# Kernel tuning notes

Hardware: AMD Instinct MI355X
Metric: run time of the kernel (lower is better)

## Reference

```python
import jax, jax.numpy as jnp
import numpy as np

B, L = 4096, 64
H, E, T, S = 512, 256, 256, 128
CT = T + 3            # context feature dim (term_embedding_dim + 3)
R, V = 4096, 256      # n production rules, n symbols
IN = 2 * E + 2 * T + 6 + H + S  # GRUCell input dim = 1670
NEG = -1e9


def setup_inputs() -> dict:
    key = jax.random.key(0)
    ks = jax.random.split(key, 24)
    sc = 0.02
    inp = {
        "s_tm1": jax.random.normal(ks[0], (B, H), jnp.float32),
        "a_tm1": jax.random.normal(ks[1], (B, E), jnp.float32),
        "p_t": jax.random.normal(ks[2], (B, H + E), jnp.float32),
        "symbol_idx": jax.random.randint(ks[3], (B,), 0, V, jnp.int32),
        "env_emb": jax.random.normal(ks[4], (B, L, CT), jnp.float32),
        "env_len": jax.random.randint(ks[5], (B,), 0, L, jnp.int32),
        "lc_emb": jax.random.normal(ks[6], (B, L, CT), jnp.float32),
        "lc_len": jax.random.randint(ks[7], (B,), 0, L, jnp.int32),
        # parameters
        "symbol_table": jax.random.normal(ks[8], (V, S), jnp.float32) * sc,
        "W1": jax.random.normal(ks[9], (H + CT, H), jnp.float32) * sc,
        "b1": jnp.zeros((H,), jnp.float32),
        "W2": jax.random.normal(ks[10], (H,), jnp.float32) * sc,
        "b2": jnp.zeros((), jnp.float32),
        "W_ih": jax.random.normal(ks[11], (IN, 3 * H), jnp.float32) * sc,
        "W_hh": jax.random.normal(ks[12], (H, 3 * H), jnp.float32) * sc,
        "b_ih": jnp.zeros((3 * H,), jnp.float32),
        "b_hh": jnp.zeros((3 * H,), jnp.float32),
        "Wd": jax.random.normal(ks[13], (H, E), jnp.float32) * sc,
        "bd": jnp.zeros((E,), jnp.float32),
        "rule_table": jax.random.normal(ks[14], (R, E), jnp.float32) * sc,
    }
    return inp


def _context_read(state, emb, length, W1, b1, W2, b2):
    # state: [B,H], emb: [B,L,CT], length: [B] -> context [B,CT]
    x = jnp.concatenate([jnp.broadcast_to(state[:, None, :], emb.shape[:2] + (state.shape[-1],)), emb], axis=-1)
    h = jax.nn.relu(jnp.einsum('blk,kh->blh', x, W1) + b1)      # [B,L,H]
    logit = jnp.einsum('blh,h->bl', h, W2) + b2                  # [B,L]
    mask = jnp.arange(emb.shape[1])[None, :] < length[:, None]
    logit = jnp.where(mask, logit, NEG)
    w = jax.nn.softmax(logit, axis=1)                            # [B,L]
    ctx = jnp.einsum('bl,blc->bc', w, emb)                       # [B,CT]
    # ragged empty-context samples use the zero default_context
    return jnp.where((length > 0)[:, None], ctx, 0.0)


def reference(s_tm1, a_tm1, p_t, symbol_idx, env_emb, env_len, lc_emb, lc_len,
              symbol_table, W1, b1, W2, b2, W_ih, W_hh, b_ih, b_hh, Wd, bd, rule_table):
    n_t = symbol_table[symbol_idx]                               # [B,S]
    ctx_env = _context_read(s_tm1, env_emb, env_len, W1, b1, W2, b2)
    ctx_lc = _context_read(s_tm1, lc_emb, lc_len, W1, b1, W2, b2)
    x = jnp.concatenate([a_tm1, p_t, n_t, ctx_env, ctx_lc], axis=-1)  # [B,IN]
    # torch GRUCell
    gx = x @ W_ih + b_ih                                         # [B,3H]
    gh = s_tm1 @ W_hh + b_hh
    xr, xz, xn = jnp.split(gx, 3, axis=-1)
    hr, hz, hn = jnp.split(gh, 3, axis=-1)
    r = jax.nn.sigmoid(xr + hr)
    z = jax.nn.sigmoid(xz + hz)
    n = jnp.tanh(xn + r * hn)
    h_new = (1.0 - z) * n + z * s_tm1                            # [B,H]
    dec = jnp.tanh(h_new @ Wd + bd)                              # [B,E]
    logits = dec @ rule_table.T                                  # [B,R]
    return logits
```

## Files before the change

kernel.cpp:

```cpp
#include <hip/hip_runtime.h>
#include <hip/hip_bf16.h>
#include <stdint.h>
#include <stddef.h>

#define XP 1696
#define KC 288
#define EP 264

#define BIG_G   8192
#define TWO_G   4096
#define ONE_G   2048
#define N_GROUP (BIG_G + TWO_G + ONE_G)
#define N_SLOTI (N_GROUP * 4)

typedef __attribute__((ext_vector_type(8))) short bf16x8;
typedef __attribute__((ext_vector_type(4))) float f32x4;

__device__ __forceinline__ unsigned short f32_bf16(float f) {
    union { float f; unsigned int u; } v; v.f = f;
    unsigned int r = v.u + 0x7FFFu + ((v.u >> 16) & 1u);
    return (unsigned short)(r >> 16);
}
__device__ __forceinline__ unsigned int bf_rnd(float f) {
    union { float f; unsigned int u; } v; v.f = f;
    return v.u + 0x7FFFu + ((v.u >> 16) & 1u);
}
__device__ __forceinline__ float bf16_f32(unsigned short u) {
    union { unsigned int u; float f; } v; v.u = ((unsigned int)u) << 16;
    return v.f;
}

__global__ void tpack_kernel(const float* __restrict__ src, unsigned short* __restrict__ dst,
                             int Ksrc, int Nsrc, int Kp) {
    __shared__ float t[64][65];
    const int tid = threadIdx.x;
    const int n0 = blockIdx.x * 64, k0 = blockIdx.y * 64;
    const int ln = tid & 63;
    const int g  = tid >> 6;
    #pragma unroll
    for (int j = 0; j < 16; j++) {
        int kl = g + j * 4;
        int k = k0 + kl, n = n0 + ln;
        float v = 0.f;
        if (k < Ksrc && n < Nsrc) v = src[(size_t)k * Nsrc + n];
        t[kl][ln] = v;
    }
    __syncthreads();
    #pragma unroll
    for (int j = 0; j < 16; j++) {
        int nl = g + j * 4;
        int n = n0 + nl, k = k0 + ln;
        if (n < Nsrc && k < Kp) dst[(size_t)n * Kp + k] = f32_bf16(t[ln][nl]);
    }
}

__global__ void cvt_kernel(const float* __restrict__ src, unsigned short* __restrict__ dst, int total) {
    int idx = blockIdx.x * blockDim.x + threadIdx.x;
    if (idx < total) dst[idx] = f32_bf16(src[idx]);
}

__global__ void xasm_kernel(const float* __restrict__ a_tm1, const float* __restrict__ p_t,
                            const int* __restrict__ sym, const float* __restrict__ symtab,
                            unsigned short* __restrict__ x_out) {
    int idx = blockIdx.x * blockDim.x + threadIdx.x;
    if (idx >= 4096 * XP) return;
    int b = idx / XP, c = idx - b * XP;
    float v;
    if (c < 256)       v = a_tm1[(size_t)b * 256 + c];
    else if (c < 1024) v = p_t[(size_t)b * 768 + (c - 256)];
    else if (c < 1152) v = symtab[(size_t)sym[b] * 128 + (c - 1024)];
    else if (c < 1670) return;
    else v = 0.0f;
    x_out[idx] = f32_bf16(v);
}

__global__ void sinit_kernel(int* __restrict__ s) {
    int i = blockIdx.x * 256 + threadIdx.x;
    if (i < N_SLOTI) s[i] = -1;
    else if (i < N_SLOTI + 3) s[i] = 0;
}

__global__ void sched_kernel(const int* __restrict__ len_env, const int* __restrict__ len_lc,
                             int* __restrict__ slots) {
    int idx = blockIdx.x * blockDim.x + threadIdx.x;
    if (idx >= 8192) return;
    int b = idx >> 1, wh = idx & 1;
    int len = wh ? len_lc[b] : len_env[b];
    int m = (len + 15) >> 4;
    if (m == 0) m = 1;
    if (m > 4) m = 4;
    int* cursors = slots + N_SLOTI;
    int base;
    if (m >= 3)      { int p = atomicAdd(&cursors[0], 1); base = p * 4; }
    else if (m == 2) { int p = atomicAdd(&cursors[1], 1); base = BIG_G * 4 + (p >> 1) * 4 + (p & 1) * 2; }
    else             { int p = atomicAdd(&cursors[2], 1); base = (BIG_G + TWO_G) * 4 + (p >> 2) * 4 + (p & 3); }
    for (int k = 0; k < m; k++) slots[base + k] = idx * 4 + k;
}

template<int ACT, int OUT_BF16>
__global__ __launch_bounds__(256, 2)
void gemm_bt_kernel(const unsigned short* __restrict__ A,
                    const unsigned short* __restrict__ BT,
                    const float* __restrict__ bias,
                    void* __restrict__ Cout,
                    int M, int N, int K)
{
    __shared__ unsigned short a_lds[128 * 32];
    __shared__ unsigned short b_lds[128 * 32];
    const int tid  = threadIdx.x;
    const int lane = tid & 63;
    const int wave = tid >> 6;
    const int wm = wave >> 1, wn = wave & 1;
    const int row0 = blockIdx.y * 128;
    const int col0 = blockIdx.x * 128;

    f32x4 acc[4][4];
    #pragma unroll
    for (int i = 0; i < 4; i++)
        #pragma unroll
        for (int j = 0; j < 4; j++) acc[i][j] = (f32x4){0.f, 0.f, 0.f, 0.f};

    const int fr = lane & 15;
    const int kk = (lane >> 4) * 8;
    const int srow = (lane >> 2);
    const int scol = (lane & 3) * 8;

    for (int k0 = 0; k0 < K; k0 += 32) {
        __syncthreads();
        #pragma unroll
        for (int j = 0; j < 4; j++) {
            const int c = (wave & 1) * 4 + j;
            const unsigned short* gsrc;
            unsigned short* ldst;
            if (wave < 2) {
                gsrc = A  + (size_t)(row0 + c * 16 + srow) * K + k0 + scol;
                ldst = &a_lds[c * 512];
            } else {
                gsrc = BT + (size_t)(col0 + c * 16 + srow) * K + k0 + scol;
                ldst = &b_lds[c * 512];
            }
            __builtin_amdgcn_global_load_lds(
                (const __attribute__((address_space(1))) void*)gsrc,
                (__attribute__((address_space(3))) void*)ldst, 16, 0, 0);
        }
        __syncthreads();

        bf16x8 af[4], bf[4];
        #pragma unroll
        for (int mt = 0; mt < 4; mt++) af[mt] = *(const bf16x8*)&a_lds[(wm * 64 + mt * 16 + fr) * 32 + kk];
        #pragma unroll
        for (int nt = 0; nt < 4; nt++) bf[nt] = *(const bf16x8*)&b_lds[(wn * 64 + nt * 16 + fr) * 32 + kk];
        #pragma unroll
        for (int mt = 0; mt < 4; mt++)
            #pragma unroll
            for (int nt = 0; nt < 4; nt++)
                acc[mt][nt] = __builtin_amdgcn_mfma_f32_16x16x32_bf16(af[mt], bf[nt], acc[mt][nt], 0, 0, 0);
    }

    const int fq = lane >> 4;
    #pragma unroll
    for (int mt = 0; mt < 4; mt++)
        #pragma unroll
        for (int nt = 0; nt < 4; nt++) {
            int cg = col0 + wn * 64 + nt * 16 + fr;
            float bv = bias ? bias[cg] : 0.0f;
            #pragma unroll
            for (int i = 0; i < 4; i++) {
                int rg = row0 + wm * 64 + mt * 16 + fq * 4 + i;
                float v = acc[mt][nt][i] + bv;
                if (ACT == 1) v = tanhf(v);
                if (OUT_BF16) ((unsigned short*)Cout)[(size_t)rg * N + cg] = f32_bf16(v);
                else          ((float*)Cout)[(size_t)rg * N + cg] = v;
            }
        }
}

__global__ __launch_bounds__(512, 4)
void ctx_kernel(const float* __restrict__ emb_env, const float* __restrict__ emb_lc,
                const int* __restrict__ len_env, const int* __restrict__ len_lc,
                const float* __restrict__ s_proj,
                const unsigned short* __restrict__ W1eT,
                const float* __restrict__ W2, const float* __restrict__ b2,
                const int* __restrict__ slots,
                unsigned short* __restrict__ x_out)
{
    const int g = blockIdx.x;
    const int4 dv = *reinterpret_cast<const int4*>(slots + (size_t)g * 4);
    if (dv.x < 0) return;
    int d[4] = {dv.x, dv.y, dv.z, dv.w};

    __shared__ unsigned short emb_lds[64 * EP];
    __shared__ float partial_lds[8][64];
    __shared__ float w_lds[64];
    __shared__ int hinfo0[4], hinfo1[4], hinfo_n;

    const int tid = threadIdx.x;
    const int lane = tid & 63;
    const int wave = tid >> 6;
    const int fr = lane & 15;
    const int fq = lane >> 4;
    const float b2v = b2[0];

    if (tid == 0) {
        int n = 0;
        #pragma unroll
        for (int s = 0; s < 4; s++) {
            int dh = d[s];
            if (dh >= 0 && (dh & 3) == 0) {
                int it = dh >> 2;
                int b = it >> 1, wh = it & 1;
                int len = (wh ? len_lc : len_env)[b];
                hinfo0[n] = (s * 16) | (len << 8);
                hinfo1[n] = b * 2 + wh;
                n++;
            }
        }
        hinfo_n = n;
    }

    if (tid < 320) {
        int r = tid / 5, c = 259 + (tid - (tid / 5) * 5);
        emb_lds[r * EP + c] = 0;
    }

    {
        const int sl = tid >> 7;
        const int t  = tid & 127;
        const int ds = d[sl];
        int nrows = 0;
        const float* src = nullptr;
        if (ds >= 0) {
            int it = ds >> 2, tix = ds & 3;
            int b = it >> 1, wh = it & 1;
            int len = (wh ? len_lc : len_env)[b];
            nrows = len - tix * 16;
            if (nrows > 16) nrows = 16;
            if (nrows < 0) nrows = 0;
            src = (wh ? emb_lc : emb_env) + ((size_t)b * 64 + tix * 16) * 259;
        }
        const int nf4 = (nrows * 259 + 3) >> 2;
        const float4* s4 = reinterpret_cast<const float4*>(src);
        float4 v[9];
        #pragma unroll
        for (int j = 0; j < 9; j++) {
            int q = t + j * 128;
            if (q < nf4) v[j] = s4[q];
        }
        unsigned short* ebase = &emb_lds[sl * 16 * EP];
        #pragma unroll
        for (int j = 0; j < 9; j++) {
            int q = t + j * 128;
            if (q < nf4) {
                int e0 = q * 4;
                int r  = (int)(((unsigned)e0 * 64779u) >> 24);
                int c0 = e0 - r * 259;
                unsigned int u0 = bf_rnd(v[j].x), u1 = bf_rnd(v[j].y);
                unsigned int u2 = bf_rnd(v[j].z), u3 = bf_rnd(v[j].w);
                unsigned short* rp = ebase + r * EP;
                if (c0 <= 255) {
                    if ((c0 & 1) == 0) {
                        *(unsigned int*)(rp + c0)     = __builtin_amdgcn_perm(u1, u0, 0x07060302);
                        *(unsigned int*)(rp + c0 + 2) = __builtin_amdgcn_perm(u3, u2, 0x07060302);
                    } else {
                        rp[c0]     = (unsigned short)(u0 >> 16);
                        *(unsigned int*)(rp + c0 + 1) = __builtin_amdgcn_perm(u2, u1, 0x07060302);
                        rp[c0 + 3] = (unsigned short)(u3 >> 16);
                    }
                } else {
                    unsigned int uu[4] = {u0, u1, u2, u3};
                    #pragma unroll
                    for (int jj = 0; jj < 4; jj++) {
                        int e = e0 + jj;
                        int r2 = r, c2 = c0 + jj;
                        if (c2 >= 259) { r2 = r + 1; c2 -= 259; }
                        ebase[r2 * EP + c2] = (unsigned short)(uu[jj] >> 16);
                    }
                }
            }
        }
    }
    __syncthreads();

    f32x4 acc[4][4];
    #pragma unroll
    for (int i = 0; i < 4; i++)
        #pragma unroll
        for (int j = 0; j < 4; j++) acc[i][j] = (f32x4){0.f, 0.f, 0.f, 0.f};

    #pragma unroll
    for (int ks = 0; ks < 9; ks++) {
        bf16x8 bfr[4];
        #pragma unroll
        for (int nt = 0; nt < 4; nt++) {
            int n = wave * 64 + nt * 16 + fr;
            bfr[nt] = *(const bf16x8*)(W1eT + (size_t)n * KC + ks * 32 + fq * 8);
        }
        bf16x8 af[4];
        if (ks < 8) {
            #pragma unroll
            for (int mt = 0; mt < 4; mt++)
                af[mt] = *(const bf16x8*)&emb_lds[(mt * 16 + fr) * EP + ks * 32 + fq * 8];
        } else {
            #pragma unroll
            for (int mt = 0; mt < 4; mt++) {
                bf16x8 z = {};
                if (fq == 0) z = *(const bf16x8*)&emb_lds[(mt * 16 + fr) * EP + 256];
                af[mt] = z;
            }
        }
        __builtin_amdgcn_s_setprio(1);
        #pragma unroll
        for (int nt = 0; nt < 4; nt++)
            #pragma unroll
            for (int mt = 0; mt < 4; mt++)
                acc[mt][nt] = __builtin_amdgcn_mfma_f32_16x16x32_bf16(af[mt], bfr[nt], acc[mt][nt], 0, 0, 0);
        __builtin_amdgcn_s_setprio(0);
    }

    int bslot[4];
    #pragma unroll
    for (int mt = 0; mt < 4; mt++) bslot[mt] = d[mt] >= 0 ? (d[mt] >> 3) : -1;

    float wv[4];
    #pragma unroll
    for (int nt = 0; nt < 4; nt++) wv[nt] = W2[wave * 64 + nt * 16 + fr];

    float plog[4][4];
    #pragma unroll
    for (int mt = 0; mt < 4; mt++)
        #pragma unroll
        for (int ii = 0; ii < 4; ii++) plog[mt][ii] = 0.f;
    #pragma unroll
    for (int nt = 0; nt < 4; nt++) {
        int n = wave * 64 + nt * 16 + fr;
        #pragma unroll
        for (int mt = 0; mt < 4; mt++) {
            if (bslot[mt] < 0) continue;
            float sp = s_proj[(size_t)bslot[mt] * 512 + n];
            #pragma unroll
            for (int ii = 0; ii < 4; ii++) {
                float h = acc[mt][nt][ii] + sp;
                h = fmaxf(h, 0.f);
                plog[mt][ii] += h * wv[nt];
            }
        }
    }
    #pragma unroll
    for (int mt = 0; mt < 4; mt++) {
        if (bslot[mt] < 0) continue;
        #pragma unroll
        for (int ii = 0; ii < 4; ii++) {
            float v = plog[mt][ii];
            v += __shfl_xor(v, 1); v += __shfl_xor(v, 2);
            v += __shfl_xor(v, 4); v += __shfl_xor(v, 8);
            if (fr == 0) partial_lds[wave][mt * 16 + fq * 4 + ii] = v;
        }
    }
    __syncthreads();

    if (wave < 4) {
        int dh = d[wave];
        if (dh >= 0 && (dh & 3) == 0) {
            int it = dh >> 2;
            int b = it >> 1, wh = it & 1;
            int len = (wh ? len_lc : len_env)[b];
            int m = (len + 15) >> 4; if (m == 0) m = 1;
            float logit = -1e9f;
            if (lane < 16 * m && lane < len) {
                logit = b2v;
                #pragma unroll
                for (int w = 0; w < 8; w++) logit += partial_lds[w][wave * 16 + lane];
            }
            float mx = logit;
            #pragma unroll
            for (int off = 1; off < 64; off <<= 1) mx = fmaxf(mx, __shfl_xor(mx, off));
            float e = __expf(logit - mx);
            float s = e;
            #pragma unroll
            for (int off = 1; off < 64; off <<= 1) s += __shfl_xor(s, off);
            if (lane < 16 * m) w_lds[wave * 16 + lane] = e / s;
        }
    }
    __syncthreads();

    {
        const int nh = hinfo_n;
        const int total = nh * 259;
        for (int q = tid; q < total; q += 512) {
            int h = (int)(((unsigned)q * 1013u) >> 18);
            int c = q - h * 259;
            int w0 = hinfo0[h];
            int base = w0 & 0xFF;
            int len = w0 >> 8;
            int w1v = hinfo1[h];
            int b = w1v >> 1, wh = w1v & 1;
            float a0 = 0.f, a1 = 0.f, a2 = 0.f, a3 = 0.f;
            int l = 0;
            for (; l + 3 < len; l += 4) {
                a0 += w_lds[base + l]     * bf16_f32(emb_lds[(base + l) * EP + c]);
                a1 += w_lds[base + l + 1] * bf16_f32(emb_lds[(base + l + 1) * EP + c]);
                a2 += w_lds[base + l + 2] * bf16_f32(emb_lds[(base + l + 2) * EP + c]);
                a3 += w_lds[base + l + 3] * bf16_f32(emb_lds[(base + l + 3) * EP + c]);
            }
            for (; l < len; l++) a0 += w_lds[base + l] * bf16_f32(emb_lds[(base + l) * EP + c]);
            x_out[(size_t)b * XP + (wh ? 1411 : 1152) + c] = f32_bf16((a0 + a1) + (a2 + a3));
        }
    }
}

__global__ void gru_kernel(const float* __restrict__ gx, const float* __restrict__ gh,
                           const float* __restrict__ s, unsigned short* __restrict__ h_b) {
    int idx = blockIdx.x * blockDim.x + threadIdx.x;
    if (idx >= 4096 * 512) return;
    int b = idx >> 9, c = idx & 511;
    const float* gxb = gx + (size_t)b * 1536;
    const float* ghb = gh + (size_t)b * 1536;
    float xr = gxb[c], xz = gxb[c + 512], xn = gxb[c + 1024];
    float hr = ghb[c], hz = ghb[c + 512], hn = ghb[c + 1024];
    float r = 1.f / (1.f + __expf(-(xr + hr)));
    float z = 1.f / (1.f + __expf(-(xz + hz)));
    float n = tanhf(xn + r * hn);
    float h = (1.f - z) * n + z * s[idx];
    h_b[idx] = f32_bf16(h);
}

extern "C" void kernel_launch(void* const* d_in, const int* in_sizes, int n_in,
                              void* d_out, int out_size, void* d_ws, size_t ws_size,
                              hipStream_t stream) {
    const float* s_tm1   = (const float*)d_in[0];
    const float* a_tm1   = (const float*)d_in[1];
    const float* p_t     = (const float*)d_in[2];
    const int*   sym     = (const int*)d_in[3];
    const float* env_emb = (const float*)d_in[4];
    const int*   env_len = (const int*)d_in[5];
    const float* lc_emb  = (const float*)d_in[6];
    const int*   lc_len  = (const int*)d_in[7];
    const float* symtab  = (const float*)d_in[8];
    const float* W1      = (const float*)d_in[9];
    const float* b1      = (const float*)d_in[10];
    const float* W2      = (const float*)d_in[11];
    const float* b2      = (const float*)d_in[12];
    const float* W_ih    = (const float*)d_in[13];
    const float* W_hh    = (const float*)d_in[14];
    const float* b_ih    = (const float*)d_in[15];
    const float* b_hh    = (const float*)d_in[16];
    const float* Wd      = (const float*)d_in[17];
    const float* bd      = (const float*)d_in[18];
    const float* rule    = (const float*)d_in[19];

    char* w = (char*)d_ws;
    float* s_proj = (float*)w;              w += (size_t)4096 * 512 * 4;
    unsigned short* W1sT  = (unsigned short*)w; w += (size_t)512 * 512 * 2;
    unsigned short* W1eT  = (unsigned short*)w; w += (size_t)512 * KC * 2;
    unsigned short* WihT  = (unsigned short*)w; w += (size_t)1536 * XP * 2;
    unsigned short* WhhT  = (unsigned short*)w; w += (size_t)1536 * 512 * 2;
    unsigned short* WdT   = (unsigned short*)w; w += (size_t)256 * 512 * 2;
    unsigned short* ruleb = (unsigned short*)w; w += (size_t)4096 * 256 * 2;
    unsigned short* s_b   = (unsigned short*)w; w += (size_t)4096 * 512 * 2;
    unsigned short* x_b   = (unsigned short*)w; w += (size_t)4096 * XP * 2;
    unsigned short* h_b   = (unsigned short*)w; w += (size_t)4096 * 512 * 2;
    unsigned short* dec_b = (unsigned short*)w; w += (size_t)4096 * 256 * 2;
    int* slots = (int*)w;                   w += (size_t)(N_SLOTI + 8) * 4;

    float* out_f = (float*)d_out;
    float* gx = out_f;
    float* gh = out_f + (size_t)4096 * 1536;

    sinit_kernel<<<(N_SLOTI + 3 + 255) / 256, 256, 0, stream>>>(slots);
    sched_kernel<<<32, 256, 0, stream>>>(env_len, lc_len, slots);

    tpack_kernel<<<dim3(8, 8),   256, 0, stream>>>(W1, W1sT, 512, 512, 512);
    tpack_kernel<<<dim3(8, 5),   256, 0, stream>>>(W1 + (size_t)512 * 512, W1eT, 259, 512, KC);
    tpack_kernel<<<dim3(24, 27), 256, 0, stream>>>(W_ih, WihT, 1670, 1536, XP);
    tpack_kernel<<<dim3(24, 8),  256, 0, stream>>>(W_hh, WhhT, 512, 1536, 512);
    tpack_kernel<<<dim3(4, 8),   256, 0, stream>>>(Wd, WdT, 512, 256, 512);
    cvt_kernel<<<4096, 256, 0, stream>>>(rule, ruleb, 4096 * 256);
    cvt_kernel<<<8192, 256, 0, stream>>>(s_tm1, s_b, 4096 * 512);
    xasm_kernel<<<(4096 * XP + 255) / 256, 256, 0, stream>>>(a_tm1, p_t, sym, symtab, x_b);

    gemm_bt_kernel<0, 0><<<dim3(4, 32), 256, 0, stream>>>(s_b, W1sT, b1, s_proj, 4096, 512, 512);

    ctx_kernel<<<N_GROUP, 512, 0, stream>>>(env_emb, lc_emb, env_len, lc_len,
                                            s_proj, W1eT, W2, b2, slots, x_b);

    gemm_bt_kernel<0, 0><<<dim3(12, 32), 256, 0, stream>>>(x_b, WihT, b_ih, gx, 4096, 1536, XP);
    gemm_bt_kernel<0, 0><<<dim3(12, 32), 256, 0, stream>>>(s_b, WhhT, b_hh, gh, 4096, 1536, 512);
    gru_kernel<<<8192, 256, 0, stream>>>(gx, gh, s_tm1, h_b);

    gemm_bt_kernel<1, 1><<<dim3(2, 32), 256, 0, stream>>>(h_b, WdT, bd, dec_b, 4096, 256, 512);

    gemm_bt_kernel<0, 0><<<dim3(32, 32), 256, 0, stream>>>(dec_b, ruleb, nullptr, out_f, 4096, 4096, 256);
}
```

Before: 463.2 us.

## Make context kernel persistent with compacted group schedule and prefetch next group

The scheduler becomes a three-pass count/base/place scheme that packs the ctx work groups contiguously, replacing fixed bucket regions that left many empty slots. The ctx kernel now runs as a persistent grid of 1024 workgroups that loop over the compacted groups. Each workgroup issues the global loads for the next group's embeddings into registers while it does the softmax and weighted sum for the current group, so memory latency overlaps compute. The cost is two extra tiny launches, higher register pressure from the prefetch buffers, and an extra barrier per iteration.

```diff
diff --git a/kernel.cpp b/kernel.cpp
--- a/kernel.cpp
+++ b/kernel.cpp
@@ -6,12 +6,9 @@
 #define XP 1696
 #define KC 288
 #define EP 264
-
-#define BIG_G   8192
-#define TWO_G   4096
-#define ONE_G   2048
-#define N_GROUP (BIG_G + TWO_G + ONE_G)
-#define N_SLOTI (N_GROUP * 4)
+#define MAXG 8192
+#define CURS_OFF (MAXG * 4)
+#define NCTX_WG 1024
 
 typedef __attribute__((ext_vector_type(8))) short bf16x8;
 typedef __attribute__((ext_vector_type(4))) float f32x4;
@@ -76,12 +73,12 @@
 
 __global__ void sinit_kernel(int* __restrict__ s) {
     int i = blockIdx.x * 256 + threadIdx.x;
-    if (i < N_SLOTI) s[i] = -1;
-    else if (i < N_SLOTI + 3) s[i] = 0;
-}
-
-__global__ void sched_kernel(const int* __restrict__ len_env, const int* __restrict__ len_lc,
-                             int* __restrict__ slots) {
+    if (i < CURS_OFF) s[i] = -1;
+    else if (i < CURS_OFF + 8) s[i] = 0;
+}
+
+__global__ void scount_kernel(const int* __restrict__ len_env, const int* __restrict__ len_lc,
+                              int* __restrict__ slots, int* __restrict__ itemrank) {
     int idx = blockIdx.x * blockDim.x + threadIdx.x;
     if (idx >= 8192) return;
     int b = idx >> 1, wh = idx & 1;
@@ -89,11 +86,37 @@
     int m = (len + 15) >> 4;
     if (m == 0) m = 1;
     if (m > 4) m = 4;
-    int* cursors = slots + N_SLOTI;
+    int bucket = (m >= 3) ? 0 : (m == 2 ? 1 : 2);
+    int* cursors = slots + CURS_OFF;
+    int rank = atomicAdd(&cursors[bucket], 1);
+    itemrank[idx] = (rank << 2) | bucket;
+}
+
+__global__ void sbase_kernel(int* __restrict__ slots) {
+    int* c = slots + CURS_OFF;
+    int nBig = c[0], nTwo = c[1], nOne = c[2];
+    int b1 = nBig;
+    int b2 = nBig + ((nTwo + 1) >> 1);
+    c[3] = 0; c[4] = b1; c[5] = b2;
+    c[6] = b2 + ((nOne + 3) >> 2);
+}
+
+__global__ void splace_kernel(const int* __restrict__ len_env, const int* __restrict__ len_lc,
+                              const int* __restrict__ itemrank, int* __restrict__ slots) {
+    int idx = blockIdx.x * blockDim.x + threadIdx.x;
+    if (idx >= 8192) return;
+    int b = idx >> 1, wh = idx & 1;
+    int len = wh ? len_lc[b] : len_env[b];
+    int m = (len + 15) >> 4;
+    if (m == 0) m = 1;
+    if (m > 4) m = 4;
+    int v = itemrank[idx];
+    int bucket = v & 3, rank = v >> 2;
+    const int* c = slots + CURS_OFF;
     int base;
-    if (m >= 3)      { int p = atomicAdd(&cursors[0], 1); base = p * 4; }
-    else if (m == 2) { int p = atomicAdd(&cursors[1], 1); base = BIG_G * 4 + (p >> 1) * 4 + (p & 1) * 2; }
-    else             { int p = atomicAdd(&cursors[2], 1); base = (BIG_G + TWO_G) * 4 + (p >> 2) * 4 + (p & 3); }
+    if (bucket == 0)      base = (c[3] + rank) * 4;
+    else if (bucket == 1) base = (c[4] + (rank >> 1)) * 4 + (rank & 1) * 2;
+    else                  base = (c[5] + (rank >> 2)) * 4 + (rank & 3);
     for (int k = 0; k < m; k++) slots[base + k] = idx * 4 + k;
 }
 
@@ -184,228 +207,260 @@
                 const int* __restrict__ slots,
                 unsigned short* __restrict__ x_out)
 {
-    const int g = blockIdx.x;
-    const int4 dv = *reinterpret_cast<const int4*>(slots + (size_t)g * 4);
-    if (dv.x < 0) return;
-    int d[4] = {dv.x, dv.y, dv.z, dv.w};
-
     __shared__ unsigned short emb_lds[64 * EP];
     __shared__ float partial_lds[8][64];
     __shared__ float w_lds[64];
-    __shared__ int hinfo0[4], hinfo1[4], hinfo_n;
-
-    const int tid = threadIdx.x;
+    __shared__ int hd[4], hlen[4], hinfo0[4], hinfo1[4], hinfo_n;
+
+    const int tid  = threadIdx.x;
     const int lane = tid & 63;
     const int wave = tid >> 6;
     const int fr = lane & 15;
     const int fq = lane >> 4;
+    const int sl = tid >> 7;
+    const int t128 = tid & 127;
     const float b2v = b2[0];
 
-    if (tid == 0) {
-        int n = 0;
-        #pragma unroll
-        for (int s = 0; s < 4; s++) {
-            int dh = d[s];
-            if (dh >= 0 && (dh & 3) == 0) {
-                int it = dh >> 2;
-                int b = it >> 1, wh = it & 1;
-                int len = (wh ? len_lc : len_env)[b];
-                hinfo0[n] = (s * 16) | (len << 8);
-                hinfo1[n] = b * 2 + wh;
-                n++;
-            }
-        }
-        hinfo_n = n;
-    }
+    float wv[4];
+    #pragma unroll
+    for (int nt = 0; nt < 4; nt++) wv[nt] = W2[wave * 64 + nt * 16 + fr];
 
     if (tid < 320) {
         int r = tid / 5, c = 259 + (tid - (tid / 5) * 5);
         emb_lds[r * EP + c] = 0;
     }
 
+    const int ng = slots[CURS_OFF + 6];
+    int g = blockIdx.x;
+    if (g >= ng) return;
+
+    float4 sv0, sv1, sv2, sv3, sv4, sv5, sv6, sv7, sv8;
+    int snf4, mylen;
+    int4 sd;
+
+#define STAGE_ISSUE(DS)                                                        \
+    {                                                                          \
+        int nrows = 0; const float* src = nullptr;                             \
+        if ((DS) >= 0) {                                                       \
+            int it = (DS) >> 2, tix = (DS) & 3;                                \
+            int bb = it >> 1, wh = it & 1;                                     \
+            mylen = (wh ? len_lc : len_env)[bb];                               \
+            nrows = mylen - tix * 16;                                          \
+            nrows = nrows < 0 ? 0 : (nrows > 16 ? 16 : nrows);                 \
+            src = (wh ? emb_lc : emb_env) + ((size_t)bb * 64 + tix * 16) * 259;\
+        } else mylen = -1;                                                     \
+        snf4 = (nrows * 259 + 3) >> 2;                                         \
+        const float4* s4 = reinterpret_cast<const float4*>(src);               \
+        if (t128 + 0 * 128 < snf4) sv0 = s4[t128 + 0 * 128];                   \
+        if (t128 + 1 * 128 < snf4) sv1 = s4[t128 + 1 * 128];                   \
+        if (t128 + 2 * 128 < snf4) sv2 = s4[t128 + 2 * 128];                   \
+        if (t128 + 3 * 128 < snf4) sv3 = s4[t128 + 3 * 128];                   \
+        if (t128 + 4 * 128 < snf4) sv4 = s4[t128 + 4 * 128];                   \
+        if (t128 + 5 * 128 < snf4) sv5 = s4[t128 + 5 * 128];                   \
+        if (t128 + 6 * 128 < snf4) sv6 = s4[t128 + 6 * 128];                   \
+        if (t128 + 7 * 128 < snf4) sv7 = s4[t128 + 7 * 128];                   \
+        if (t128 + 8 * 128 < snf4) sv8 = s4[t128 + 8 * 128];                   \
+    }
+
+#define ST_ONE(VJ, J)                                                          \
+    { int q = t128 + (J) * 128;                                                \
+      if (q < snf4) {                                                          \
+        int e0 = q * 4;                                                        \
+        int r  = (int)(((unsigned)e0 * 64779u) >> 24);                         \
+        int c0 = e0 - r * 259;                                                 \
+        unsigned u0 = bf_rnd(VJ.x), u1 = bf_rnd(VJ.y);                         \
+        unsigned u2 = bf_rnd(VJ.z), u3 = bf_rnd(VJ.w);                         \
+        unsigned short* rp = ebase + r * EP;                                   \
+        if (c0 <= 255) {                                                       \
+            if ((c0 & 1) == 0) {                                               \
+                *(unsigned int*)(rp + c0)     = __builtin_amdgcn_perm(u1, u0, 0x07060302); \
+                *(unsigned int*)(rp + c0 + 2) = __builtin_amdgcn_perm(u3, u2, 0x07060302); \
+            } else {                                                           \
+                rp[c0]     = (unsigned short)(u0 >> 16);                       \
+                *(unsigned int*)(rp + c0 + 1) = __builtin_amdgcn_perm(u2, u1, 0x07060302); \
+                rp[c0 + 3] = (unsigned short)(u3 >> 16);                       \
+            }                                                                  \
+        } else {                                                               \
+            unsigned uu[4] = {u0, u1, u2, u3};                                 \
+            _Pragma("unroll")                                                  \
+            for (int jj = 0; jj < 4; jj++) {                                   \
+                int e = e0 + jj;                                               \
+                int r2 = r, c2 = c0 + jj;                                      \
+                if (c2 >= 259) { r2 = r + 1; c2 -= 259; }                      \
+                ebase[r2 * EP + c2] = (unsigned short)(uu[jj] >> 16);          \
+            }                                                                  \
+        } } }
+
+    sd = *reinterpret_cast<const int4*>(slots + (size_t)g * 4);
     {
-        const int sl = tid >> 7;
-        const int t  = tid & 127;
-        const int ds = d[sl];
-        int nrows = 0;
-        const float* src = nullptr;
-        if (ds >= 0) {
-            int it = ds >> 2, tix = ds & 3;
-            int b = it >> 1, wh = it & 1;
-            int len = (wh ? len_lc : len_env)[b];
-            nrows = len - tix * 16;
-            if (nrows > 16) nrows = 16;
-            if (nrows < 0) nrows = 0;
-            src = (wh ? emb_lc : emb_env) + ((size_t)b * 64 + tix * 16) * 259;
-        }
-        const int nf4 = (nrows * 259 + 3) >> 2;
-        const float4* s4 = reinterpret_cast<const float4*>(src);
-        float4 v[9];
-        #pragma unroll
-        for (int j = 0; j < 9; j++) {
-            int q = t + j * 128;
-            if (q < nf4) v[j] = s4[q];
-        }
-        unsigned short* ebase = &emb_lds[sl * 16 * EP];
-        #pragma unroll
-        for (int j = 0; j < 9; j++) {
-            int q = t + j * 128;
-            if (q < nf4) {
-                int e0 = q * 4;
-                int r  = (int)(((unsigned)e0 * 64779u) >> 24);
-                int c0 = e0 - r * 259;
-                unsigned int u0 = bf_rnd(v[j].x), u1 = bf_rnd(v[j].y);
-                unsigned int u2 = bf_rnd(v[j].z), u3 = bf_rnd(v[j].w);
-                unsigned short* rp = ebase + r * EP;
-                if (c0 <= 255) {
-                    if ((c0 & 1) == 0) {
-                        *(unsigned int*)(rp + c0)     = __builtin_amdgcn_perm(u1, u0, 0x07060302);
-                        *(unsigned int*)(rp + c0 + 2) = __builtin_amdgcn_perm(u3, u2, 0x07060302);
-                    } else {
-                        rp[c0]     = (unsigned short)(u0 >> 16);
-                        *(unsigned int*)(rp + c0 + 1) = __builtin_amdgcn_perm(u2, u1, 0x07060302);
-                        rp[c0 + 3] = (unsigned short)(u3 >> 16);
-                    }
-                } else {
-                    unsigned int uu[4] = {u0, u1, u2, u3};
-                    #pragma unroll
-                    for (int jj = 0; jj < 4; jj++) {
-                        int e = e0 + jj;
-                        int r2 = r, c2 = c0 + jj;
-                        if (c2 >= 259) { r2 = r + 1; c2 -= 259; }
-                        ebase[r2 * EP + c2] = (unsigned short)(uu[jj] >> 16);
-                    }
+        int ds = (sl == 0) ? sd.x : (sl == 1) ? sd.y : (sl == 2) ? sd.z : sd.w;
+        STAGE_ISSUE(ds);
+    }
+
+    for (;;) {
+        {
+            unsigned short* ebase = &emb_lds[sl * 16 * EP];
+            ST_ONE(sv0, 0) ST_ONE(sv1, 1) ST_ONE(sv2, 2) ST_ONE(sv3, 3)
+            ST_ONE(sv4, 4) ST_ONE(sv5, 5) ST_ONE(sv6, 6) ST_ONE(sv7, 7)
+            ST_ONE(sv8, 8)
+        }
+        if (t128 == 0) {
+            int ds = (sl == 0) ? sd.x : (sl == 1) ? sd.y : (sl == 2) ? sd.z : sd.w;
+            hd[sl] = ds; hlen[sl] = mylen;
+        }
+        __syncthreads();
+
+        int bs[4];
+        bs[0] = sd.x >= 0 ? (sd.x >> 3) : -1;
+        bs[1] = sd.y >= 0 ? (sd.y >> 3) : -1;
+        bs[2] = sd.z >= 0 ? (sd.z >> 3) : -1;
+        bs[3] = sd.w >= 0 ? (sd.w >> 3) : -1;
+
+        if (tid == 0) {
+            int n = 0;
+            #pragma unroll
+            for (int s = 0; s < 4; s++) {
+                int dh = hd[s];
+                if (dh >= 0 && (dh & 3) == 0) {
+                    hinfo0[n] = (s * 16) | (hlen[s] << 8);
+                    hinfo1[n] = (dh >> 3) * 2 + ((dh >> 2) & 1);
+                    n++;
                 }
             }
-        }
-    }
-    __syncthreads();
-
-    f32x4 acc[4][4];
-    #pragma unroll
-    for (int i = 0; i < 4; i++)
-        #pragma unroll
-        for (int j = 0; j < 4; j++) acc[i][j] = (f32x4){0.f, 0.f, 0.f, 0.f};
-
-    #pragma unroll
-    for (int ks = 0; ks < 9; ks++) {
-        bf16x8 bfr[4];
+            hinfo_n = n;
+        }
+
+        f32x4 acc[4][4];
+        #pragma unroll
+        for (int i = 0; i < 4; i++)
+            #pragma unroll
+            for (int j = 0; j < 4; j++) acc[i][j] = (f32x4){0.f, 0.f, 0.f, 0.f};
+
+        #pragma unroll
+        for (int ks = 0; ks < 9; ks++) {
+            bf16x8 bfr[4];
+            #pragma unroll
+            for (int nt = 0; nt < 4; nt++) {
+                int n = wave * 64 + nt * 16 + fr;
+                bfr[nt] = *(const bf16x8*)(W1eT + (size_t)n * KC + ks * 32 + fq * 8);
+            }
+            bf16x8 af[4];
+            if (ks < 8) {
+                #pragma unroll
+                for (int mt = 0; mt < 4; mt++)
+                    af[mt] = *(const bf16x8*)&emb_lds[(mt * 16 + fr) * EP + ks * 32 + fq * 8];
+            } else {
+                #pragma unroll
+                for (int mt = 0; mt < 4; mt++) {
+                    bf16x8 z = {};
+                    if (fq == 0) z = *(const bf16x8*)&emb_lds[(mt * 16 + fr) * EP + 256];
+                    af[mt] = z;
+                }
+            }
+            __builtin_amdgcn_s_setprio(1);
+            #pragma unroll
+            for (int nt = 0; nt < 4; nt++)
+                #pragma unroll
+                for (int mt = 0; mt < 4; mt++)
+                    acc[mt][nt] = __builtin_amdgcn_mfma_f32_16x16x32_bf16(af[mt], bfr[nt], acc[mt][nt], 0, 0, 0);
+            __builtin_amdgcn_s_setprio(0);
+        }
+
+        float plog[4][4];
+        #pragma unroll
+        for (int mt = 0; mt < 4; mt++)
+            #pragma unroll
+            for (int ii = 0; ii < 4; ii++) plog[mt][ii] = 0.f;
         #pragma unroll
         for (int nt = 0; nt < 4; nt++) {
             int n = wave * 64 + nt * 16 + fr;
-            bfr[nt] = *(const bf16x8*)(W1eT + (size_t)n * KC + ks * 32 + fq * 8);
-        }
-        bf16x8 af[4];
-        if (ks < 8) {
-            #pragma unroll
-            for (int mt = 0; mt < 4; mt++)
-                af[mt] = *(const bf16x8*)&emb_lds[(mt * 16 + fr) * EP + ks * 32 + fq * 8];
-        } else {
             #pragma unroll
             for (int mt = 0; mt < 4; mt++) {
-                bf16x8 z = {};
-                if (fq == 0) z = *(const bf16x8*)&emb_lds[(mt * 16 + fr) * EP + 256];
-                af[mt] = z;
-            }
-        }
-        __builtin_amdgcn_s_setprio(1);
-        #pragma unroll
-        for (int nt = 0; nt < 4; nt++)
-            #pragma unroll
-            for (int mt = 0; mt < 4; mt++)
-                acc[mt][nt] = __builtin_amdgcn_mfma_f32_16x16x32_bf16(af[mt], bfr[nt], acc[mt][nt], 0, 0, 0);
-        __builtin_amdgcn_s_setprio(0);
-    }
-
-    int bslot[4];
-    #pragma unroll
-    for (int mt = 0; mt < 4; mt++) bslot[mt] = d[mt] >= 0 ? (d[mt] >> 3) : -1;
-
-    float wv[4];
-    #pragma unroll
-    for (int nt = 0; nt < 4; nt++) wv[nt] = W2[wave * 64 + nt * 16 + fr];
-
-    float plog[4][4];
-    #pragma unroll
-    for (int mt = 0; mt < 4; mt++)
-        #pragma unroll
-        for (int ii = 0; ii < 4; ii++) plog[mt][ii] = 0.f;
-    #pragma unroll
-    for (int nt = 0; nt < 4; nt++) {
-        int n = wave * 64 + nt * 16 + fr;
+                if (bs[mt] < 0) continue;
+                float sp = s_proj[(size_t)bs[mt] * 512 + n];
+                #pragma unroll
+                for (int ii = 0; ii < 4; ii++) {
+                    float h = acc[mt][nt][ii] + sp;
+                    h = fmaxf(h, 0.f);
+                    plog[mt][ii] += h * wv[nt];
+                }
+            }
+        }
+
+        const int gn = g + NCTX_WG;
+        const bool more = (gn < ng);
+        if (more) {
+            sd = *reinterpret_cast<const int4*>(slots + (size_t)gn * 4);
+            int ds = (sl == 0) ? sd.x : (sl == 1) ? sd.y : (sl == 2) ? sd.z : sd.w;
+            STAGE_ISSUE(ds);
+        }
+
         #pragma unroll
         for (int mt = 0; mt < 4; mt++) {
-            if (bslot[mt] < 0) continue;
-            float sp = s_proj[(size_t)bslot[mt] * 512 + n];
+            if (bs[mt] < 0) continue;
             #pragma unroll
             for (int ii = 0; ii < 4; ii++) {
-                float h = acc[mt][nt][ii] + sp;
-                h = fmaxf(h, 0.f);
-                plog[mt][ii] += h * wv[nt];
-            }
-        }
-    }
-    #pragma unroll
-    for (int mt = 0; mt < 4; mt++) {
-        if (bslot[mt] < 0) continue;
-        #pragma unroll
-        for (int ii = 0; ii < 4; ii++) {
-            float v = plog[mt][ii];
-            v += __shfl_xor(v, 1); v += __shfl_xor(v, 2);
-            v += __shfl_xor(v, 4); v += __shfl_xor(v, 8);
-            if (fr == 0) partial_lds[wave][mt * 16 + fq * 4 + ii] = v;
-        }
-    }
-    __syncthreads();
-
-    if (wave < 4) {
-        int dh = d[wave];
-        if (dh >= 0 && (dh & 3) == 0) {
-            int it = dh >> 2;
-            int b = it >> 1, wh = it & 1;
-            int len = (wh ? len_lc : len_env)[b];
-            int m = (len + 15) >> 4; if (m == 0) m = 1;
-            float logit = -1e9f;
-            if (lane < 16 * m && lane < len) {
-                logit = b2v;
+                float v = plog[mt][ii];
+                v += __shfl_xor(v, 1); v += __shfl_xor(v, 2);
+                v += __shfl_xor(v, 4); v += __shfl_xor(v, 8);
+                if (fr == 0) partial_lds[wave][mt * 16 + fq * 4 + ii] = v;
+            }
+        }
+        __syncthreads();
+
+        if (wave < 4) {
+            int dh = hd[wave];
+            if (dh >= 0 && (dh & 3) == 0) {
+                int len = hlen[wave];
+                int m = (len + 15) >> 4; if (m == 0) m = 1;
+                float logit = -1e9f;
+                if (lane < 16 * m && lane < len) {
+                    logit = b2v;
+                    #pragma unroll
+                    for (int w = 0; w < 8; w++) logit += partial_lds[w][wave * 16 + lane];
+                }
+                float mx = logit;
                 #pragma unroll
-                for (int w = 0; w < 8; w++) logit += partial_lds[w][wave * 16 + lane];
-            }
-            float mx = logit;
-            #pragma unroll
-            for (int off = 1; off < 64; off <<= 1) mx = fmaxf(mx, __shfl_xor(mx, off));
-            float e = __expf(logit - mx);
-            float s = e;
-            #pragma unroll
-            for (int off = 1; off < 64; off <<= 1) s += __shfl_xor(s, off);
-            if (lane < 16 * m) w_lds[wave * 16 + lane] = e / s;
-        }
-    }
-    __syncthreads();
-
-    {
-        const int nh = hinfo_n;
-        const int total = nh * 259;
-        for (int q = tid; q < total; q += 512) {
-            int h = (int)(((unsigned)q * 1013u) >> 18);
-            int c = q - h * 259;
-            int w0 = hinfo0[h];
-            int base = w0 & 0xFF;
-            int len = w0 >> 8;
-            int w1v = hinfo1[h];
-            int b = w1v >> 1, wh = w1v & 1;
-            float a0 = 0.f, a1 = 0.f, a2 = 0.f, a3 = 0.f;
-            int l = 0;
-            for (; l + 3 < len; l += 4) {
-                a0 += w_lds[base + l]     * bf16_f32(emb_lds[(base + l) * EP + c]);
-                a1 += w_lds[base + l + 1] * bf16_f32(emb_lds[(base + l + 1) * EP + c]);
-                a2 += w_lds[base + l + 2] * bf16_f32(emb_lds[(base + l + 2) * EP + c]);
-                a3 += w_lds[base + l + 3] * bf16_f32(emb_lds[(base + l + 3) * EP + c]);
-            }
-            for (; l < len; l++) a0 += w_lds[base + l] * bf16_f32(emb_lds[(base + l) * EP + c]);
-            x_out[(size_t)b * XP + (wh ? 1411 : 1152) + c] = f32_bf16((a0 + a1) + (a2 + a3));
-        }
-    }
+                for (int off = 1; off < 64; off <<= 1) mx = fmaxf(mx, __shfl_xor(mx, off));
+                float e = __expf(logit - mx);
+                float s = e;
+                #pragma unroll
+                for (int off = 1; off < 64; off <<= 1) s += __shfl_xor(s, off);
+                if (lane < 16 * m) w_lds[wave * 16 + lane] = e / s;
+            }
+        }
+        __syncthreads();
+
+        {
+            const int nh = hinfo_n;
+            const int total = nh * 259;
+            for (int q = tid; q < total; q += 512) {
+                int h = (int)(((unsigned)q * 1013u) >> 18);
+                int c = q - h * 259;
+                int w0 = hinfo0[h];
+                int base = w0 & 0xFF;
+                int len = w0 >> 8;
+                int w1v = hinfo1[h];
+                int b = w1v >> 1, wh = w1v & 1;
+                float a0 = 0.f, a1 = 0.f, a2 = 0.f, a3 = 0.f;
+                int l = 0;
+                for (; l + 3 < len; l += 4) {
+                    a0 += w_lds[base + l]     * bf16_f32(emb_lds[(base + l) * EP + c]);
+                    a1 += w_lds[base + l + 1] * bf16_f32(emb_lds[(base + l + 1) * EP + c]);
+                    a2 += w_lds[base + l + 2] * bf16_f32(emb_lds[(base + l + 2) * EP + c]);
+                    a3 += w_lds[base + l + 3] * bf16_f32(emb_lds[(base + l + 3) * EP + c]);
+                }
+                for (; l < len; l++) a0 += w_lds[base + l] * bf16_f32(emb_lds[(base + l) * EP + c]);
+                x_out[(size_t)b * XP + (wh ? 1411 : 1152) + c] = f32_bf16((a0 + a1) + (a2 + a3));
+            }
+        }
+        __syncthreads();
+
+        if (!more) break;
+        g = gn;
+    }
+#undef STAGE_ISSUE
+#undef ST_ONE
 }
 
 __global__ void gru_kernel(const float* __restrict__ gx, const float* __restrict__ gh,
@@ -460,14 +515,17 @@
     unsigned short* x_b   = (unsigned short*)w; w += (size_t)4096 * XP * 2;
     unsigned short* h_b   = (unsigned short*)w; w += (size_t)4096 * 512 * 2;
     unsigned short* dec_b = (unsigned short*)w; w += (size_t)4096 * 256 * 2;
-    int* slots = (int*)w;                   w += (size_t)(N_SLOTI + 8) * 4;
+    int* slots    = (int*)w;                w += (size_t)(CURS_OFF + 8) * 4;
+    int* itemrank = (int*)w;                w += (size_t)8192 * 4;
 
     float* out_f = (float*)d_out;
     float* gx = out_f;
     float* gh = out_f + (size_t)4096 * 1536;
 
-    sinit_kernel<<<(N_SLOTI + 3 + 255) / 256, 256, 0, stream>>>(slots);
-    sched_kernel<<<32, 256, 0, stream>>>(env_len, lc_len, slots);
+    sinit_kernel<<<(CURS_OFF + 8 + 255) / 256, 256, 0, stream>>>(slots);
+    scount_kernel<<<32, 256, 0, stream>>>(env_len, lc_len, slots, itemrank);
+    sbase_kernel<<<1, 1, 0, stream>>>(slots);
+    splace_kernel<<<32, 256, 0, stream>>>(env_len, lc_len, itemrank, slots);
 
     tpack_kernel<<<dim3(8, 8),   256, 0, stream>>>(W1, W1sT, 512, 512, 512);
     tpack_kernel<<<dim3(8, 5),   256, 0, stream>>>(W1 + (size_t)512 * 512, W1eT, 259, 512, KC);
@@ -480,7 +538,7 @@
 
     gemm_bt_kernel<0, 0><<<dim3(4, 32), 256, 0, stream>>>(s_b, W1sT, b1, s_proj, 4096, 512, 512);
 
-    ctx_kernel<<<N_GROUP, 512, 0, stream>>>(env_emb, lc_emb, env_len, lc_len,
+    ctx_kernel<<<NCTX_WG, 512, 0, stream>>>(env_emb, lc_emb, env_len, lc_len,
                                             s_proj, W1eT, W2, b2, slots, x_b);
 
     gemm_bt_kernel<0, 0><<<dim3(12, 32), 256, 0, stream>>>(x_b, WihT, b_ih, gx, 4096, 1536, XP);
```

Result: slower. 1.480 ms (+219.6%).

## Compact ctx scheduling, double K-tile in GEMM, prefetch W1e fragments

Applied to the files above, without the earlier changes.

The scheduler becomes count/prefix/place passes so context groups are packed densely and ctx_kernel blocks beyond the live group count exit immediately, where before 14336 mostly-empty block slots were launched. The generic GEMM now stages a 64-wide K tile per barrier pair, halving synchronisations, and XP is padded to a multiple of 64 to match. ctx_kernel also software-prefetches the next W1e fragment ahead of the MFMAs. The cost is more LDS per GEMM block, which may limit occupancy, plus two extra small launches.

```diff
diff --git a/kernel.cpp b/kernel.cpp
--- a/kernel.cpp
+++ b/kernel.cpp
@@ -3,15 +3,11 @@
 #include <stdint.h>
 #include <stddef.h>
 
-#define XP 1696
+#define XP 1728
 #define KC 288
 #define EP 264
-
-#define BIG_G   8192
-#define TWO_G   4096
-#define ONE_G   2048
-#define N_GROUP (BIG_G + TWO_G + ONE_G)
-#define N_SLOTI (N_GROUP * 4)
+#define MAXG 8192
+#define CURS_OFF (MAXG * 4)
 
 typedef __attribute__((ext_vector_type(8))) short bf16x8;
 typedef __attribute__((ext_vector_type(4))) float f32x4;
@@ -76,12 +72,12 @@
 
 __global__ void sinit_kernel(int* __restrict__ s) {
     int i = blockIdx.x * 256 + threadIdx.x;
-    if (i < N_SLOTI) s[i] = -1;
-    else if (i < N_SLOTI + 3) s[i] = 0;
-}
-
-__global__ void sched_kernel(const int* __restrict__ len_env, const int* __restrict__ len_lc,
-                             int* __restrict__ slots) {
+    if (i < CURS_OFF) s[i] = -1;
+    else if (i < CURS_OFF + 8) s[i] = 0;
+}
+
+__global__ void scount_kernel(const int* __restrict__ len_env, const int* __restrict__ len_lc,
+                              int* __restrict__ slots, int* __restrict__ itemrank) {
     int idx = blockIdx.x * blockDim.x + threadIdx.x;
     if (idx >= 8192) return;
     int b = idx >> 1, wh = idx & 1;
@@ -89,11 +85,37 @@
     int m = (len + 15) >> 4;
     if (m == 0) m = 1;
     if (m > 4) m = 4;
-    int* cursors = slots + N_SLOTI;
+    int bucket = (m >= 3) ? 0 : (m == 2 ? 1 : 2);
+    int* cursors = slots + CURS_OFF;
+    int rank = atomicAdd(&cursors[bucket], 1);
+    itemrank[idx] = (rank << 2) | bucket;
+}
+
+__global__ void sbase_kernel(int* __restrict__ slots) {
+    int* c = slots + CURS_OFF;
+    int nBig = c[0], nTwo = c[1], nOne = c[2];
+    int b1 = nBig;
+    int b2 = nBig + ((nTwo + 1) >> 1);
+    c[3] = 0; c[4] = b1; c[5] = b2;
+    c[6] = b2 + ((nOne + 3) >> 2);
+}
+
+__global__ void splace_kernel(const int* __restrict__ len_env, const int* __restrict__ len_lc,
+                              const int* __restrict__ itemrank, int* __restrict__ slots) {
+    int idx = blockIdx.x * blockDim.x + threadIdx.x;
+    if (idx >= 8192) return;
+    int b = idx >> 1, wh = idx & 1;
+    int len = wh ? len_lc[b] : len_env[b];
+    int m = (len + 15) >> 4;
+    if (m == 0) m = 1;
+    if (m > 4) m = 4;
+    int v = itemrank[idx];
+    int bucket = v & 3, rank = v >> 2;
+    const int* c = slots + CURS_OFF;
     int base;
-    if (m >= 3)      { int p = atomicAdd(&cursors[0], 1); base = p * 4; }
-    else if (m == 2) { int p = atomicAdd(&cursors[1], 1); base = BIG_G * 4 + (p >> 1) * 4 + (p & 1) * 2; }
-    else             { int p = atomicAdd(&cursors[2], 1); base = (BIG_G + TWO_G) * 4 + (p >> 2) * 4 + (p & 3); }
+    if (bucket == 0)      base = (c[3] + rank) * 4;
+    else if (bucket == 1) base = (c[4] + (rank >> 1)) * 4 + (rank & 1) * 2;
+    else                  base = (c[5] + (rank >> 2)) * 4 + (rank & 3);
     for (int k = 0; k < m; k++) slots[base + k] = idx * 4 + k;
 }
 
@@ -105,8 +127,8 @@
                     void* __restrict__ Cout,
                     int M, int N, int K)
 {
-    __shared__ unsigned short a_lds[128 * 32];
-    __shared__ unsigned short b_lds[128 * 32];
+    __shared__ unsigned short a_lds[128 * 64];
+    __shared__ unsigned short b_lds[128 * 64];
     const int tid  = threadIdx.x;
     const int lane = tid & 63;
     const int wave = tid >> 6;
@@ -121,22 +143,23 @@
         for (int j = 0; j < 4; j++) acc[i][j] = (f32x4){0.f, 0.f, 0.f, 0.f};
 
     const int fr = lane & 15;
-    const int kk = (lane >> 4) * 8;
-    const int srow = (lane >> 2);
-    const int scol = (lane & 3) * 8;
-
-    for (int k0 = 0; k0 < K; k0 += 32) {
+    const int fq = lane >> 4;
+    const int srow8 = lane >> 3;
+    const int scol  = (lane & 7) * 8;
+
+    for (int k0 = 0; k0 < K; k0 += 64) {
         __syncthreads();
         #pragma unroll
-        for (int j = 0; j < 4; j++) {
-            const int c = (wave & 1) * 4 + j;
+        for (int j = 0; j < 8; j++) {
+            const int c = (wave & 1) * 8 + j;
+            const int row = c * 8 + srow8;
             const unsigned short* gsrc;
             unsigned short* ldst;
             if (wave < 2) {
-                gsrc = A  + (size_t)(row0 + c * 16 + srow) * K + k0 + scol;
+                gsrc = A  + (size_t)(row0 + row) * K + k0 + scol;
                 ldst = &a_lds[c * 512];
             } else {
-                gsrc = BT + (size_t)(col0 + c * 16 + srow) * K + k0 + scol;
+                gsrc = BT + (size_t)(col0 + row) * K + k0 + scol;
                 ldst = &b_lds[c * 512];
             }
             __builtin_amdgcn_global_load_lds(
@@ -145,19 +168,23 @@
         }
         __syncthreads();
 
-        bf16x8 af[4], bf[4];
-        #pragma unroll
-        for (int mt = 0; mt < 4; mt++) af[mt] = *(const bf16x8*)&a_lds[(wm * 64 + mt * 16 + fr) * 32 + kk];
-        #pragma unroll
-        for (int nt = 0; nt < 4; nt++) bf[nt] = *(const bf16x8*)&b_lds[(wn * 64 + nt * 16 + fr) * 32 + kk];
-        #pragma unroll
-        for (int mt = 0; mt < 4; mt++)
+        #pragma unroll
+        for (int h = 0; h < 2; h++) {
+            bf16x8 af[4], bf[4];
+            #pragma unroll
+            for (int mt = 0; mt < 4; mt++)
+                af[mt] = *(const bf16x8*)&a_lds[(wm * 64 + mt * 16 + fr) * 64 + h * 32 + fq * 8];
             #pragma unroll
             for (int nt = 0; nt < 4; nt++)
-                acc[mt][nt] = __builtin_amdgcn_mfma_f32_16x16x32_bf16(af[mt], bf[nt], acc[mt][nt], 0, 0, 0);
-    }
-
-    const int fq = lane >> 4;
+                bf[nt] = *(const bf16x8*)&b_lds[(wn * 64 + nt * 16 + fr) * 64 + h * 32 + fq * 8];
+            #pragma unroll
+            for (int mt = 0; mt < 4; mt++)
+                #pragma unroll
+                for (int nt = 0; nt < 4; nt++)
+                    acc[mt][nt] = __builtin_amdgcn_mfma_f32_16x16x32_bf16(af[mt], bf[nt], acc[mt][nt], 0, 0, 0);
+        }
+    }
+
     #pragma unroll
     for (int mt = 0; mt < 4; mt++)
         #pragma unroll
@@ -184,9 +211,10 @@
                 const int* __restrict__ slots,
                 unsigned short* __restrict__ x_out)
 {
+    const int ng = slots[CURS_OFF + 6];
     const int g = blockIdx.x;
+    if (g >= ng) return;
     const int4 dv = *reinterpret_cast<const int4*>(slots + (size_t)g * 4);
-    if (dv.x < 0) return;
     int d[4] = {dv.x, dv.y, dv.z, dv.w};
 
     __shared__ unsigned short emb_lds[64 * EP];
@@ -207,11 +235,10 @@
         for (int s = 0; s < 4; s++) {
             int dh = d[s];
             if (dh >= 0 && (dh & 3) == 0) {
-                int it = dh >> 2;
-                int b = it >> 1, wh = it & 1;
-                int len = (wh ? len_lc : len_env)[b];
+                int bb = dh >> 3, wh = (dh >> 2) & 1;
+                int len = (wh ? len_lc : len_env)[bb];
                 hinfo0[n] = (s * 16) | (len << 8);
-                hinfo1[n] = b * 2 + wh;
+                hinfo1[n] = bb * 2 + wh;
                 n++;
             }
         }
@@ -279,6 +306,13 @@
             }
         }
     }
+
+    bf16x8 bcur[4];
+    #pragma unroll
+    for (int nt = 0; nt < 4; nt++) {
+        int n = wave * 64 + nt * 16 + fr;
+        bcur[nt] = *(const bf16x8*)(W1eT + (size_t)n * KC + 0 + fq * 8);
+    }
     __syncthreads();
 
     f32x4 acc[4][4];
@@ -289,11 +323,13 @@
 
     #pragma unroll
     for (int ks = 0; ks < 9; ks++) {
-        bf16x8 bfr[4];
-        #pragma unroll
-        for (int nt = 0; nt < 4; nt++) {
-            int n = wave * 64 + nt * 16 + fr;
-            bfr[nt] = *(const bf16x8*)(W1eT + (size_t)n * KC + ks * 32 + fq * 8);
+        bf16x8 bnxt[4];
+        if (ks < 8) {
+            #pragma unroll
+            for (int nt = 0; nt < 4; nt++) {
+                int n = wave * 64 + nt * 16 + fr;
+                bnxt[nt] = *(const bf16x8*)(W1eT + (size_t)n * KC + (ks + 1) * 32 + fq * 8);
+            }
         }
         bf16x8 af[4];
         if (ks < 8) {
@@ -313,8 +349,12 @@
         for (int nt = 0; nt < 4; nt++)
             #pragma unroll
             for (int mt = 0; mt < 4; mt++)
-                acc[mt][nt] = __builtin_amdgcn_mfma_f32_16x16x32_bf16(af[mt], bfr[nt], acc[mt][nt], 0, 0, 0);
+                acc[mt][nt] = __builtin_amdgcn_mfma_f32_16x16x32_bf16(af[mt], bcur[nt], acc[mt][nt], 0, 0, 0);
         __builtin_amdgcn_s_setprio(0);
+        if (ks < 8) {
+            #pragma unroll
+            for (int nt = 0; nt < 4; nt++) bcur[nt] = bnxt[nt];
+        }
     }
 
     int bslot[4];
@@ -361,9 +401,8 @@
     if (wave < 4) {
         int dh = d[wave];
         if (dh >= 0 && (dh & 3) == 0) {
-            int it = dh >> 2;
-            int b = it >> 1, wh = it & 1;
-            int len = (wh ? len_lc : len_env)[b];
+            int bb = dh >> 3, wh = (dh >> 2) & 1;
+            int len = (wh ? len_lc : len_env)[bb];
             int m = (len + 15) >> 4; if (m == 0) m = 1;
             float logit = -1e9f;
             if (lane < 16 * m && lane < len) {
@@ -460,14 +499,17 @@
     unsigned short* x_b   = (unsigned short*)w; w += (size_t)4096 * XP * 2;
     unsigned short* h_b   = (unsigned short*)w; w += (size_t)4096 * 512 * 2;
     unsigned short* dec_b = (unsigned short*)w; w += (size_t)4096 * 256 * 2;
-    int* slots = (int*)w;                   w += (size_t)(N_SLOTI + 8) * 4;
+    int* slots    = (int*)w;                w += (size_t)(CURS_OFF + 8) * 4;
+    int* itemrank = (int*)w;                w += (size_t)8192 * 4;
 
     float* out_f = (float*)d_out;
     float* gx = out_f;
     float* gh = out_f + (size_t)4096 * 1536;
 
-    sinit_kernel<<<(N_SLOTI + 3 + 255) / 256, 256, 0, stream>>>(slots);
-    sched_kernel<<<32, 256, 0, stream>>>(env_len, lc_len, slots);
+    sinit_kernel<<<(CURS_OFF + 8 + 255) / 256, 256, 0, stream>>>(slots);
+    scount_kernel<<<32, 256, 0, stream>>>(env_len, lc_len, slots, itemrank);
+    sbase_kernel<<<1, 1, 0, stream>>>(slots);
+    splace_kernel<<<32, 256, 0, stream>>>(env_len, lc_len, itemrank, slots);
 
     tpack_kernel<<<dim3(8, 8),   256, 0, stream>>>(W1, W1sT, 512, 512, 512);
     tpack_kernel<<<dim3(8, 5),   256, 0, stream>>>(W1 + (size_t)512 * 512, W1eT, 259, 512, KC);
@@ -480,8 +522,8 @@
 
     gemm_bt_kernel<0, 0><<<dim3(4, 32), 256, 0, stream>>>(s_b, W1sT, b1, s_proj, 4096, 512, 512);
 
-    ctx_kernel<<<N_GROUP, 512, 0, stream>>>(env_emb, lc_emb, env_len, lc_len,
-                                            s_proj, W1eT, W2, b2, slots, x_b);
+    ctx_kernel<<<MAXG, 512, 0, stream>>>(env_emb, lc_emb, env_len, lc_len,
+                                         s_proj, W1eT, W2, b2, slots, x_b);
 
     gemm_bt_kernel<0, 0><<<dim3(12, 32), 256, 0, stream>>>(x_b, WihT, b_ih, gx, 4096, 1536, XP);
     gemm_bt_kernel<0, 0><<<dim3(12, 32), 256, 0, stream>>>(s_b, WhhT, b_hh, gh, 4096, 1536, 512);
```

Result: slower. 566.5 us (+22.3%).
